# Performance work log

Measured on AMD Instinct MI355X. Metric: run time of the kernel, lower is better.

Reference implementation:

```python
import jax, jax.numpy as jnp
import numpy as np

EPS = 1e-06


def setup_inputs() -> dict:
    key = jax.random.key(0)
    k1, k2 = jax.random.split(key)
    B, T, E = 4, 4096, 1024
    M = E // 2
    x = jax.random.normal(k1, (B, T, E), dtype=jnp.float32)
    # causal mask: position i may attend to j <= i... note module multiplies K
    # (which is nonzero only for j >= i) by mask; a standard causal lower-tri
    # mask would zero everything but the diagonal. The module's bump kernel
    # looks FORWARD (diff = (j-i).clamp(min=0)), so the natural mask here is
    # upper-triangular (j >= i), i.e. the 'causal' mask for this pooling.
    mask = jnp.triu(jnp.ones((T, T), dtype=bool))
    gate_raw = jnp.full((M,), -3.0, dtype=jnp.float32)
    return {"x": x, "mask": mask, "gate_raw": gate_raw}


def reference(x, mask, gate_raw):
    B, T, E = x.shape
    dtype = x.dtype
    x_c = x[..., 0::2]                                  # (B, T, M) content channels

    # convex bump kernel K[i, j], nonzero for j >= i
    i = jnp.arange(T, dtype=dtype)[:, None]
    j = jnp.arange(T, dtype=dtype)[None, :]
    diff = jnp.maximum(j - i, 0.0)
    horizon = jnp.maximum(jnp.float32(T) - i, 1.0)
    u = jnp.minimum(diff / horizon, 1.0 - EPS)
    K = jnp.exp(1.0 - 1.0 / (1.0 - u * u + EPS))
    K = jnp.where(u >= 1.0 - EPS, jnp.asarray(EPS, dtype), K)

    K = K * mask.astype(dtype)
    K = K / jnp.maximum(K.sum(-1, keepdims=True), EPS)  # row-normalize

    phi = jnp.einsum('ij,bjm->bim', K, x_c)             # (B, T, M)
    gate = jax.nn.softplus(gate_raw)[None, None, :]     # (1, 1, M)
    out = x.at[..., 1::2].set(phi * gate)               # write phase channels
    return out
```

## Files before the change

kernel.cpp:

```cpp
#include <hip/hip_runtime.h>
#include <cstdint>
#include <cstddef>

#define Tdim 4096
#define Bdim 4
#define Edim 1024
#define Mdim 512
#define EPSF 1e-6f

typedef __bf16 bf16x8 __attribute__((ext_vector_type(8)));
typedef float f32x4 __attribute__((ext_vector_type(4)));

__device__ __forceinline__ unsigned short f2bf(float f) {
  union { float f; unsigned int u; } a; a.f = f;
  unsigned int r = a.u + 0x7fffu + ((a.u >> 16) & 1u);
  return (unsigned short)(r >> 16);
}

__device__ __forceinline__ float kernel_g(float dj, float inv_h) {
  float u = fminf(dj * inv_h, 1.0f - EPSF);
  return __expf(1.0f - 1.0f / (1.0f - u * u + EPSF));
}

typedef void __attribute__((address_space(1)))* gas1;
typedef void __attribute__((address_space(3)))* las3;
__device__ __forceinline__ void load_lds16(const void* g, void* l) {
  __builtin_amdgcn_global_load_lds((gas1)(g), (las3)(l), 16, 0, 0);
}


__global__ __launch_bounds__(256) void gate_kernel(const float* __restrict__ graw,
                                                   float* __restrict__ gate) {
  const int m = blockIdx.x * 256 + threadIdx.x;
  if (m < Mdim) {
    const float v = graw[m];
    gate[m] = fmaxf(v, 0.0f) + log1pf(__expf(-fabsf(v)));
  }
}

__global__ __launch_bounds__(256) void rowsum_kernel(float* __restrict__ inv_rowsum) {
  const int i = blockIdx.x;
  const int tid = threadIdx.x;
  const float inv_h = 1.0f / (float)(Tdim - i);
  float s = 0.0f;
  for (int j = i + tid; j < Tdim; j += 256)
    s += kernel_g((float)(j - i), inv_h);
#pragma unroll
  for (int off = 32; off; off >>= 1) s += __shfl_down(s, off);
  __shared__ float red[4];
  if ((tid & 63) == 0) red[tid >> 6] = s;
  __syncthreads();
  if (tid == 0) inv_rowsum[i] = 1.0f / (red[0] + red[1] + red[2] + red[3]);
}

__global__ __launch_bounds__(256) void kgen_kernel(const float* __restrict__ inv_rowsum,
                                                   unsigned short* __restrict__ Kmat) {
  const int i = blockIdx.y;
  const int j0 = (blockIdx.x * 256 + threadIdx.x) * 8;
  union { unsigned short u[8]; uint4 v; } pk;
  if (j0 + 7 < i) {
    pk.v = make_uint4(0u, 0u, 0u, 0u);
  } else {
    const float inv_h = 1.0f / (float)(Tdim - i);
    const float inv_s = inv_rowsum[i];
#pragma unroll
    for (int t = 0; t < 8; ++t) {
      const int j = j0 + t;
      float r = 0.0f;
      if (j >= i) r = kernel_g((float)(j - i), inv_h) * inv_s;
      pk.u[t] = f2bf(r);
    }
  }
  *reinterpret_cast<uint4*>(&Kmat[(size_t)i * Tdim + j0]) = pk.v;
}

__global__ __launch_bounds__(256) void extract_kernel(const float* __restrict__ x,
                                                      unsigned short* __restrict__ XcT) {
  __shared__ unsigned short Ls[32][68];
  const int j0 = blockIdx.x * 64;
  const int m0 = blockIdx.y * 32;
  const int b  = blockIdx.z;
  const int tid = threadIdx.x;
  const int q = tid & 15;
  const int jbase = tid >> 4;
#pragma unroll
  for (int it = 0; it < 4; ++it) {
    const int jj = jbase + it * 16;
    const size_t off = ((size_t)(b * Tdim + j0 + jj)) * Edim + 2 * m0 + 4 * q;
    const float4 v = *reinterpret_cast<const float4*>(&x[off]);
    Ls[2 * q][jj]     = f2bf(v.x);
    Ls[2 * q + 1][jj] = f2bf(v.z);
  }
  __syncthreads();
  const int ch = tid & 15;
  const int mb = tid >> 4;
#pragma unroll
  for (int it = 0; it < 2; ++it) {
    const int m = mb + it * 16;
    ushort4 uv;
    uv.x = Ls[m][4 * ch];
    uv.y = Ls[m][4 * ch + 1];
    uv.z = Ls[m][4 * ch + 2];
    uv.w = Ls[m][4 * ch + 3];
    *reinterpret_cast<ushort4*>(
        &XcT[((size_t)(b * Mdim + m0 + m)) * Tdim + j0 + 4 * ch]) = uv;
  }
}

__global__ __launch_bounds__(256) void gemm_kernel(
    const unsigned short* __restrict__ Kmat,
    const unsigned short* __restrict__ XcT,
    const float* __restrict__ x,
    const float* __restrict__ gate,
    float* __restrict__ out) {
  const int i0 = blockIdx.x * 128;
  const int m0 = blockIdx.y * 128;
  const int b  = blockIdx.z;
  __shared__ unsigned short As[128 * 64];
  __shared__ unsigned short Bs[128 * 64];
  const int tid = threadIdx.x;
  const int w = tid >> 6;
  const int l = tid & 63;
  f32x4 acc[4][4] = {};
  const int wr = w >> 1, wc = w & 1;
  const unsigned short* Arow = Kmat + (size_t)i0 * Tdim;
  const unsigned short* Brow = XcT + ((size_t)b * Mdim + m0) * Tdim;
  const int srow = l >> 3;
  const int scol = (l & 7) * 8;

  for (int j0 = i0; j0 < Tdim; j0 += 64) {
#pragma unroll
    for (int t = 0; t < 4; ++t) {
      const int rr = (w * 4 + t) * 8 + srow;
      load_lds16(Arow + (size_t)rr * Tdim + (j0 + scol), &As[(w * 4 + t) * 512]);
      load_lds16(Brow + (size_t)rr * Tdim + (j0 + scol), &Bs[(w * 4 + t) * 512]);
    }
    __syncthreads();
    const int lr16 = l & 15;
    const int kq = (l >> 4) * 8;
#pragma unroll
    for (int kk = 0; kk < 2; ++kk) {
      bf16x8 af[4], bfr[4];
      const int k0 = kk * 32 + kq;
#pragma unroll
      for (int r = 0; r < 4; ++r)
        af[r] = *reinterpret_cast<const bf16x8*>(&As[(wr * 64 + r * 16 + lr16) * 64 + k0]);
#pragma unroll
      for (int c = 0; c < 4; ++c)
        bfr[c] = *reinterpret_cast<const bf16x8*>(&Bs[(wc * 64 + c * 16 + lr16) * 64 + k0]);
#pragma unroll
      for (int r = 0; r < 4; ++r)
#pragma unroll
        for (int c = 0; c < 4; ++c)
          acc[r][c] = __builtin_amdgcn_mfma_f32_16x16x32_bf16(af[r], bfr[c], acc[r][c], 0, 0, 0);
    }
    __syncthreads();
  }

  const int lr = l & 15;
  const int lq = l >> 4;
#pragma unroll
  for (int r = 0; r < 4; ++r) {
    const int i = i0 + wr * 64 + r * 16 + lq * 4;
#pragma unroll
    for (int c = 0; c < 4; ++c) {
      const int m = m0 + wc * 64 + c * 16 + lr;
      const float gm = gate[m];
#pragma unroll
      for (int v = 0; v < 4; ++v) {
        const size_t o = ((size_t)(b * Tdim + i + v)) * Edim + 2 * m;
        const float2 xv = *reinterpret_cast<const float2*>(&x[o]);
        float2 res;
        res.x = xv.x;
        res.y = acc[r][c][v] * gm;
        *reinterpret_cast<float2*>(&out[o]) = res;
      }
    }
  }
}

__global__ __launch_bounds__(256) void fallback_kernel(const float* __restrict__ x,
                                                       const float* __restrict__ graw,
                                                       float* __restrict__ out) {
  const int i = blockIdx.x, b = blockIdx.y, tid = threadIdx.x;
  const float inv_h = 1.0f / (float)(Tdim - i);
  float s = 0.0f;
  for (int j = i + tid; j < Tdim; j += 256)
    s += kernel_g((float)(j - i), inv_h);
#pragma unroll
  for (int off = 32; off; off >>= 1) s += __shfl_down(s, off);
  __shared__ float red[4];
  __shared__ float sinv_sh;
  if ((tid & 63) == 0) red[tid >> 6] = s;
  __syncthreads();
  if (tid == 0) sinv_sh = 1.0f / (red[0] + red[1] + red[2] + red[3]);
  __syncthreads();
  const float sinv = sinv_sh;
  const float* xb = x + (size_t)b * Tdim * Edim;
  float a0 = 0.0f, a1 = 0.0f;
  const int m0 = tid, m1 = tid + 256;
  for (int j = i; j < Tdim; ++j) {
    const float wgt = kernel_g((float)(j - i), inv_h);
    const float* xr = xb + (size_t)j * Edim;
    a0 += wgt * xr[2 * m0];
    a1 += wgt * xr[2 * m1];
  }
  const float v0 = graw[m0], v1 = graw[m1];
  const float g0 = fmaxf(v0, 0.0f) + log1pf(__expf(-fabsf(v0)));
  const float g1 = fmaxf(v1, 0.0f) + log1pf(__expf(-fabsf(v1)));
  const size_t o = ((size_t)(b * Tdim + i)) * Edim;
  const float* xi = xb + (size_t)i * Edim;
  out[o + 2 * m0]     = xi[2 * m0];
  out[o + 2 * m0 + 1] = a0 * sinv * g0;
  out[o + 2 * m1]     = xi[2 * m1];
  out[o + 2 * m1 + 1] = a1 * sinv * g1;
}

extern "C" void kernel_launch(void* const* d_in, const int* in_sizes, int n_in,
                              void* d_out, int out_size, void* d_ws, size_t ws_size,
                              hipStream_t stream) {
  const float* x = (const float*)d_in[0];
  const float* gate_raw = (const float*)d_in[2];
  float* out = (float*)d_out;

  const size_t XcT_bytes = (size_t)Bdim * Mdim * Tdim * 2;
  const size_t K_bytes   = (size_t)Tdim * Tdim * 2;
  const size_t need = XcT_bytes + K_bytes + (size_t)(Tdim + Mdim) * sizeof(float);

  if (ws_size < need) {
    fallback_kernel<<<dim3(Tdim, Bdim), 256, 0, stream>>>(x, gate_raw, out);
    return;
  }

  char* ws = (char*)d_ws;
  unsigned short* XcT  = (unsigned short*)ws;
  unsigned short* Kmat = (unsigned short*)(ws + XcT_bytes);
  float* inv_rowsum    = (float*)(ws + XcT_bytes + K_bytes);
  float* gate          = inv_rowsum + Tdim;

  gate_kernel<<<dim3((Mdim + 255) / 256), 256, 0, stream>>>(gate_raw, gate);
  rowsum_kernel<<<dim3(Tdim), 256, 0, stream>>>(inv_rowsum);
  kgen_kernel<<<dim3(Tdim / (256 * 8), Tdim), 256, 0, stream>>>(inv_rowsum, Kmat);
  extract_kernel<<<dim3(Tdim / 64, Mdim / 32, Bdim), 256, 0, stream>>>(x, XcT);
  gemm_kernel<<<dim3(Tdim / 128, Mdim / 128, Bdim), 256, 0, stream>>>(Kmat, XcT, x, gate, out);
}
```

Measured before the change: 259.3 us.

## Split-K the triangular GEMM with atomics and swizzle LDS layout

The GEMM grid is reshaped so each row block's triangular K range is split into 1024-wide chunks. This balances work across blocks, since early row blocks previously did far more iterations than late ones. Partial results go via float atomicAdd into a zeroed fp32 phi buffer, and a new finalize kernel writes the interleaved output with the gate applied. LDS accesses are also XOR-swizzled to reduce bank conflicts. The cost is an extra memset, atomic traffic, and a full extra pass over x and phi.

```diff
diff --git a/kernel.cpp b/kernel.cpp
--- a/kernel.cpp
+++ b/kernel.cpp
@@ -110,12 +110,18 @@
 __global__ __launch_bounds__(256) void gemm_kernel(
     const unsigned short* __restrict__ Kmat,
     const unsigned short* __restrict__ XcT,
-    const float* __restrict__ x,
-    const float* __restrict__ gate,
-    float* __restrict__ out) {
-  const int i0 = blockIdx.x * 128;
+    float* __restrict__ phi) {
+  int bx = blockIdx.x;
+  int p = 0;
+  int nc = 4;
+  while (bx >= nc) { bx -= nc; ++p; nc = (64 - 2 * p + 15) >> 4; }
+  const int q = bx;
+  const int i0 = p * 128;
   const int m0 = blockIdx.y * 128;
   const int b  = blockIdx.z;
+  const int jstart = i0 + q * 1024;
+  const int jend   = min(jstart + 1024, Tdim);
+
   __shared__ unsigned short As[128 * 64];
   __shared__ unsigned short Bs[128 * 64];
   const int tid = threadIdx.x;
@@ -125,29 +131,31 @@
   const int wr = w >> 1, wc = w & 1;
   const unsigned short* Arow = Kmat + (size_t)i0 * Tdim;
   const unsigned short* Brow = XcT + ((size_t)b * Mdim + m0) * Tdim;
-  const int srow = l >> 3;
-  const int scol = (l & 7) * 8;
-
-  for (int j0 = i0; j0 < Tdim; j0 += 64) {
+  const int srow  = l >> 3;
+  const int sslot = l & 7;
+  const int schunk = (sslot ^ srow) * 8;
+
+  for (int j0 = jstart; j0 < jend; j0 += 64) {
 #pragma unroll
     for (int t = 0; t < 4; ++t) {
       const int rr = (w * 4 + t) * 8 + srow;
-      load_lds16(Arow + (size_t)rr * Tdim + (j0 + scol), &As[(w * 4 + t) * 512]);
-      load_lds16(Brow + (size_t)rr * Tdim + (j0 + scol), &Bs[(w * 4 + t) * 512]);
+      load_lds16(Arow + (size_t)rr * Tdim + (j0 + schunk), &As[(w * 4 + t) * 512]);
+      load_lds16(Brow + (size_t)rr * Tdim + (j0 + schunk), &Bs[(w * 4 + t) * 512]);
     }
     __syncthreads();
     const int lr16 = l & 15;
-    const int kq = (l >> 4) * 8;
+    const int kq = l >> 4;
 #pragma unroll
     for (int kk = 0; kk < 2; ++kk) {
       bf16x8 af[4], bfr[4];
-      const int k0 = kk * 32 + kq;
+      const int chunk = kk * 4 + kq;
+      const int slot = (chunk ^ (lr16 & 7)) * 8;
 #pragma unroll
       for (int r = 0; r < 4; ++r)
-        af[r] = *reinterpret_cast<const bf16x8*>(&As[(wr * 64 + r * 16 + lr16) * 64 + k0]);
+        af[r] = *reinterpret_cast<const bf16x8*>(&As[(wr * 64 + r * 16 + lr16) * 64 + slot]);
 #pragma unroll
       for (int c = 0; c < 4; ++c)
-        bfr[c] = *reinterpret_cast<const bf16x8*>(&Bs[(wc * 64 + c * 16 + lr16) * 64 + k0]);
+        bfr[c] = *reinterpret_cast<const bf16x8*>(&Bs[(wc * 64 + c * 16 + lr16) * 64 + slot]);
 #pragma unroll
       for (int r = 0; r < 4; ++r)
 #pragma unroll
@@ -165,18 +173,31 @@
 #pragma unroll
     for (int c = 0; c < 4; ++c) {
       const int m = m0 + wc * 64 + c * 16 + lr;
-      const float gm = gate[m];
-#pragma unroll
-      for (int v = 0; v < 4; ++v) {
-        const size_t o = ((size_t)(b * Tdim + i + v)) * Edim + 2 * m;
-        const float2 xv = *reinterpret_cast<const float2*>(&x[o]);
-        float2 res;
-        res.x = xv.x;
-        res.y = acc[r][c][v] * gm;
-        *reinterpret_cast<float2*>(&out[o]) = res;
-      }
-    }
-  }
+#pragma unroll
+      for (int v = 0; v < 4; ++v)
+        atomicAdd(&phi[((size_t)(b * Tdim + i + v)) * Mdim + m], acc[r][c][v]);
+    }
+  }
+}
+
+__global__ __launch_bounds__(256) void finalize_kernel(const float* __restrict__ x,
+                                                       const float* __restrict__ phi,
+                                                       const float* __restrict__ gate,
+                                                       float* __restrict__ out) {
+  const size_t idx = (size_t)blockIdx.x * 256 + threadIdx.x;
+  const size_t o = idx * 4;
+  const int e = (int)(o & (size_t)(Edim - 1));
+  const size_t bt = o >> 10;
+  const int m = e >> 1;
+  const float4 xv = *reinterpret_cast<const float4*>(&x[o]);
+  const float2 ph = *reinterpret_cast<const float2*>(&phi[bt * Mdim + m]);
+  const float2 g  = *reinterpret_cast<const float2*>(&gate[m]);
+  float4 r;
+  r.x = xv.x;
+  r.y = ph.x * g.x;
+  r.z = xv.z;
+  r.w = ph.y * g.y;
+  *reinterpret_cast<float4*>(&out[o]) = r;
 }
 
 __global__ __launch_bounds__(256) void fallback_kernel(const float* __restrict__ x,
@@ -225,7 +246,9 @@
 
   const size_t XcT_bytes = (size_t)Bdim * Mdim * Tdim * 2;
   const size_t K_bytes   = (size_t)Tdim * Tdim * 2;
-  const size_t need = XcT_bytes + K_bytes + (size_t)(Tdim + Mdim) * sizeof(float);
+  const size_t phi_bytes = (size_t)Bdim * Tdim * Mdim * sizeof(float);
+  const size_t need = XcT_bytes + K_bytes + phi_bytes +
+                      (size_t)(Tdim + Mdim) * sizeof(float);
 
   if (ws_size < need) {
     fallback_kernel<<<dim3(Tdim, Bdim), 256, 0, stream>>>(x, gate_raw, out);
@@ -235,12 +258,15 @@
   char* ws = (char*)d_ws;
   unsigned short* XcT  = (unsigned short*)ws;
   unsigned short* Kmat = (unsigned short*)(ws + XcT_bytes);
-  float* inv_rowsum    = (float*)(ws + XcT_bytes + K_bytes);
+  float* phi           = (float*)(ws + XcT_bytes + K_bytes);
+  float* inv_rowsum    = (float*)(ws + XcT_bytes + K_bytes + phi_bytes);
   float* gate          = inv_rowsum + Tdim;
 
+  hipMemsetAsync(phi, 0, phi_bytes, stream);
   gate_kernel<<<dim3((Mdim + 255) / 256), 256, 0, stream>>>(gate_raw, gate);
   rowsum_kernel<<<dim3(Tdim), 256, 0, stream>>>(inv_rowsum);
   kgen_kernel<<<dim3(Tdim / (256 * 8), Tdim), 256, 0, stream>>>(inv_rowsum, Kmat);
   extract_kernel<<<dim3(Tdim / 64, Mdim / 32, Bdim), 256, 0, stream>>>(x, XcT);
-  gemm_kernel<<<dim3(Tdim / 128, Mdim / 128, Bdim), 256, 0, stream>>>(Kmat, XcT, x, gate, out);
-}
+  gemm_kernel<<<dim3(80, Mdim / 128, Bdim), 256, 0, stream>>>(Kmat, XcT, phi);
+  finalize_kernel<<<dim3((Bdim * Tdim * Edim) / 4 / 256), 256, 0, stream>>>(x, phi, gate, out);
+}
```

Result: slower. 282.9 us (+9.1%).

## Double-buffer LDS tiles in GEMM and XOR-swizzle LDS layout

Applied to the files above, without the earlier changes.

The GEMM main loop now keeps two LDS buffers per operand, so the global-to-LDS loads for the next K-tile are issued while MFMAs run on the current one. This removes one barrier per iteration. Each lane's global chunk is also XOR-swizzled by row when staged, and the fragment reads apply the same XOR, to reduce LDS bank conflicts on the 16-byte reads. LDS use doubles to 64 KB per block, which may lower occupancy, and a single barrier per iteration must be enough to protect buffer reuse.

```diff
diff --git a/kernel.cpp b/kernel.cpp
--- a/kernel.cpp
+++ b/kernel.cpp
@@ -113,11 +113,13 @@
     const float* __restrict__ x,
     const float* __restrict__ gate,
     float* __restrict__ out) {
-  const int i0 = blockIdx.x * 128;
+  const int p  = blockIdx.x;
+  const int i0 = p * 128;
   const int m0 = blockIdx.y * 128;
   const int b  = blockIdx.z;
-  __shared__ unsigned short As[128 * 64];
-  __shared__ unsigned short Bs[128 * 64];
+
+  __shared__ unsigned short As[2][128 * 64];
+  __shared__ unsigned short Bs[2][128 * 64];
   const int tid = threadIdx.x;
   const int w = tid >> 6;
   const int l = tid & 63;
@@ -125,36 +127,48 @@
   const int wr = w >> 1, wc = w & 1;
   const unsigned short* Arow = Kmat + (size_t)i0 * Tdim;
   const unsigned short* Brow = XcT + ((size_t)b * Mdim + m0) * Tdim;
-  const int srow = l >> 3;
-  const int scol = (l & 7) * 8;
-
-  for (int j0 = i0; j0 < Tdim; j0 += 64) {
-#pragma unroll
-    for (int t = 0; t < 4; ++t) {
-      const int rr = (w * 4 + t) * 8 + srow;
-      load_lds16(Arow + (size_t)rr * Tdim + (j0 + scol), &As[(w * 4 + t) * 512]);
-      load_lds16(Brow + (size_t)rr * Tdim + (j0 + scol), &Bs[(w * 4 + t) * 512]);
-    }
+  const int srow  = l >> 3;
+  const int sslot = l & 7;
+  const int schunk = (sslot ^ srow) * 8;
+
+#pragma unroll
+  for (int t = 0; t < 4; ++t) {
+    const int rr = (w * 4 + t) * 8 + srow;
+    load_lds16(Arow + (size_t)rr * Tdim + (i0 + schunk), &As[0][(w * 4 + t) * 512]);
+    load_lds16(Brow + (size_t)rr * Tdim + (i0 + schunk), &Bs[0][(w * 4 + t) * 512]);
+  }
+
+  int cur = 0;
+  const int lr16 = l & 15;
+  const int kq = l >> 4;
+  for (int j0 = i0; j0 < Tdim; j0 += 64, cur ^= 1) {
     __syncthreads();
-    const int lr16 = l & 15;
-    const int kq = (l >> 4) * 8;
+    const int jn = j0 + 64;
+    if (jn < Tdim) {
+#pragma unroll
+      for (int t = 0; t < 4; ++t) {
+        const int rr = (w * 4 + t) * 8 + srow;
+        load_lds16(Arow + (size_t)rr * Tdim + (jn + schunk), &As[cur ^ 1][(w * 4 + t) * 512]);
+        load_lds16(Brow + (size_t)rr * Tdim + (jn + schunk), &Bs[cur ^ 1][(w * 4 + t) * 512]);
+      }
+    }
 #pragma unroll
     for (int kk = 0; kk < 2; ++kk) {
       bf16x8 af[4], bfr[4];
-      const int k0 = kk * 32 + kq;
+      const int chunk = kk * 4 + kq;
+      const int slot = (chunk ^ (lr16 & 7)) * 8;
 #pragma unroll
       for (int r = 0; r < 4; ++r)
-        af[r] = *reinterpret_cast<const bf16x8*>(&As[(wr * 64 + r * 16 + lr16) * 64 + k0]);
+        af[r] = *reinterpret_cast<const bf16x8*>(&As[cur][(wr * 64 + r * 16 + lr16) * 64 + slot]);
 #pragma unroll
       for (int c = 0; c < 4; ++c)
-        bfr[c] = *reinterpret_cast<const bf16x8*>(&Bs[(wc * 64 + c * 16 + lr16) * 64 + k0]);
+        bfr[c] = *reinterpret_cast<const bf16x8*>(&Bs[cur][(wc * 64 + c * 16 + lr16) * 64 + slot]);
 #pragma unroll
       for (int r = 0; r < 4; ++r)
 #pragma unroll
         for (int c = 0; c < 4; ++c)
           acc[r][c] = __builtin_amdgcn_mfma_f32_16x16x32_bf16(af[r], bfr[c], acc[r][c], 0, 0, 0);
     }
-    __syncthreads();
   }
 
   const int lr = l & 15;
```

Result: faster. 247.8 us (-4.4%).
